# Performance work log

Hardware: AMD Instinct MI355X
Metric: run time of the kernel (lower is better)

The kernel has to match this reference:

```python
import jax, jax.numpy as jnp
import numpy as np


def _layernorm(x, g, b, eps=1e-5):
    mu = jnp.mean(x, axis=-1, keepdims=True)
    var = jnp.mean(jnp.square(x - mu), axis=-1, keepdims=True)
    return (x - mu) * jax.lax.rsqrt(var + eps) * g + b


def setup_inputs() -> dict:
    key = jax.random.key(0)
    ks = jax.random.split(key, 8)
    dim, ctx_dim, heads, dim_head = 256, 256, 8, 64
    inner = heads * dim_head
    s = 0.02
    return {
        "x": jax.random.normal(ks[0], (4, dim, 64, 64), jnp.float32),
        "y": jax.random.normal(ks[1], (4, 1024, ctx_dim), jnp.float32),
        "ln_x_g": jnp.ones((dim,), jnp.float32),
        "ln_x_b": jnp.zeros((dim,), jnp.float32),
        "ln_y_g": jnp.ones((ctx_dim,), jnp.float32),
        "ln_y_b": jnp.zeros((ctx_dim,), jnp.float32),
        "Wq": jax.random.normal(ks[2], (dim, inner), jnp.float32) * s,
        "Wk": jax.random.normal(ks[3], (ctx_dim, inner), jnp.float32) * s,
        "Wv": jax.random.normal(ks[4], (ctx_dim, inner), jnp.float32) * s,
        "bv": jnp.zeros((inner,), jnp.float32),
        "Wo": jax.random.normal(ks[5], (inner, dim), jnp.float32) * s,
        "bo": jnp.zeros((dim,), jnp.float32),
    }


def reference(x, y, ln_x_g, ln_x_b, ln_y_g, ln_y_b, Wq, Wk, Wv, bv, Wo, bo):
    heads, dim_head = 8, 64
    b, c = x.shape[:2]
    # channel_last=False path: [b, c, H, W] -> [b, n, c]
    xn = x.reshape(b, c, -1).swapaxes(1, 2)
    xn = _layernorm(xn, ln_x_g, ln_x_b)          # note: x is reassigned in torch code
    yn = _layernorm(y, ln_y_g, ln_y_b)
    q = xn @ Wq                                   # [b, n, h*d]
    k = yn @ Wk                                   # [b, m, h*d]
    v = yn @ Wv + bv                              # [b, m, h*d]

    def split_heads(t):
        B, N, _ = t.shape
        return t.reshape(B, N, heads, dim_head).transpose(0, 2, 1, 3)  # [b, h, n, d]

    q, k, v = split_heads(q), split_heads(k), split_heads(v)
    attn = jnp.einsum("bhid,bhjd->bhij", q, k) * (dim_head ** -0.5)
    attn = jax.nn.softmax(attn, axis=-1)
    out = jnp.einsum("bhij,bhjd->bhid", attn, v)  # [b, h, n, d]
    out = out.transpose(0, 2, 1, 3).reshape(b, -1, heads * dim_head)
    out = out @ Wo + bo
    return xn + out  # residual with layernormed x (faithful to source)
```

## Files before the change

kernel.cpp:

```cpp
#include <hip/hip_runtime.h>
#include <hip/hip_bf16.h>
#include <cstddef>
#include <cstdint>

#define BATCH 4
#define CDIM 256
#define HW 4096
#define MCTX 1024
#define CTX 256
#define HEADS 8
#define DHEAD 64
#define INNER 512

typedef __attribute__((ext_vector_type(8))) short bf16x8;
typedef __attribute__((ext_vector_type(4))) float f32x4;

static __device__ __forceinline__ ushort f2bf(float f) {
  __hip_bfloat16 h = __float2bfloat16(f);
  return *reinterpret_cast<ushort*>(&h);
}

static __device__ __forceinline__ void gload16(const void* g, void* l) {
  __builtin_amdgcn_global_load_lds(
      (const __attribute__((address_space(1))) void*)(uintptr_t)g,
      (__attribute__((address_space(3))) void*)(uint32_t)(uintptr_t)l,
      16, 0, 0);
}

__global__ __launch_bounds__(256) void ln_x_kernel(
    const float* __restrict__ x, const float* __restrict__ g,
    const float* __restrict__ bta, float* __restrict__ xn,
    ushort* __restrict__ xnbf) {
  const int blk = blockIdx.x;
  const int bi = blk / (HW / 32);
  const int n0 = (blk % (HW / 32)) * 32;
  __shared__ float xt[32][257];
  __shared__ float smu[32], srs[32];
  const int t = threadIdx.x;
  const float* xb = x + (size_t)bi * CDIM * HW;
  {
    const int cr = t >> 3;
    const int n4 = (t & 7) * 4;
    #pragma unroll
    for (int pass = 0; pass < 8; ++pass) {
      const int c = pass * 32 + cr;
      float4 v = *(const float4*)(xb + (size_t)c * HW + n0 + n4);
      xt[n4 + 0][c] = v.x; xt[n4 + 1][c] = v.y;
      xt[n4 + 2][c] = v.z; xt[n4 + 3][c] = v.w;
    }
  }
  __syncthreads();
  const int col = t >> 3, j = t & 7;
  float s = 0.f, ss = 0.f;
  #pragma unroll
  for (int c = j; c < CDIM; c += 8) {
    float v = xt[col][c];
    s += v; ss += v * v;
  }
  #pragma unroll
  for (int off = 1; off < 8; off <<= 1) {
    s += __shfl_xor(s, off);
    ss += __shfl_xor(ss, off);
  }
  if (j == 0) {
    float mu = s * (1.f / CDIM);
    smu[col] = mu;
    srs[col] = rsqrtf(ss * (1.f / CDIM) - mu * mu + 1e-5f);
  }
  __syncthreads();
  const float gv = g[t], bvv = bta[t];
  float* xnb = xn + ((size_t)bi * HW + n0) * CDIM;
  ushort* xbb = xnbf + ((size_t)bi * HW + n0) * CDIM;
  #pragma unroll 4
  for (int n = 0; n < 32; ++n) {
    float val = (xt[n][t] - smu[n]) * srs[n] * gv + bvv;
    xnb[(size_t)n * CDIM + t] = val;
    xbb[(size_t)n * CDIM + t] = f2bf(val);
  }
}

__global__ __launch_bounds__(256) void ln_y_kernel(
    const float* __restrict__ y, const float* __restrict__ g,
    const float* __restrict__ bta, ushort* __restrict__ ynbf) {
  const int row = blockIdx.x * 4 + (threadIdx.x >> 6);
  const int t = threadIdx.x & 63;
  float4 v = ((const float4*)(y + (size_t)row * CTX))[t];
  float s = v.x + v.y + v.z + v.w;
  float ss = v.x * v.x + v.y * v.y + v.z * v.z + v.w * v.w;
  #pragma unroll
  for (int off = 1; off < 64; off <<= 1) {
    s += __shfl_xor(s, off);
    ss += __shfl_xor(ss, off);
  }
  float mu = s * (1.f / CTX);
  float rs = rsqrtf(ss * (1.f / CTX) - mu * mu + 1e-5f);
  float4 gv = ((const float4*)g)[t];
  float4 b4 = ((const float4*)bta)[t];
  ushort4 ob;
  ob.x = f2bf((v.x - mu) * rs * gv.x + b4.x);
  ob.y = f2bf((v.y - mu) * rs * gv.y + b4.y);
  ob.z = f2bf((v.z - mu) * rs * gv.z + b4.z);
  ob.w = f2bf((v.w - mu) * rs * gv.w + b4.w);
  *(ushort4*)(ynbf + (size_t)row * CTX + t * 4) = ob;
}

static __device__ __forceinline__ void wprep_body(
    const float* __restrict__ W, ushort* __restrict__ Wt, int K, int N,
    int bx, int by) {
  __shared__ ushort T[64][65];
  const int k0 = by * 64, n0 = bx * 64;
  const int t = threadIdx.x;
  #pragma unroll
  for (int rr = 0; rr < 4; ++rr) {
    int row = rr * 16 + (t >> 4);
    int c = (t & 15) * 4;
    float4 wv = *(const float4*)(W + (size_t)(k0 + row) * N + n0 + c);
    T[row][c + 0] = f2bf(wv.x); T[row][c + 1] = f2bf(wv.y);
    T[row][c + 2] = f2bf(wv.z); T[row][c + 3] = f2bf(wv.w);
  }
  __syncthreads();
  #pragma unroll
  for (int rr = 0; rr < 4; ++rr) {
    int nrow = rr * 16 + (t >> 4);
    int kc = (t & 15) * 4;
    ushort4 o;
    o.x = T[kc + 0][nrow]; o.y = T[kc + 1][nrow];
    o.z = T[kc + 2][nrow]; o.w = T[kc + 3][nrow];
    *(ushort4*)(Wt + (size_t)(n0 + nrow) * K + k0 + kc) = o;
  }
}

__global__ __launch_bounds__(256) void wprep4_kernel(
    const float* __restrict__ W0, const float* __restrict__ W1,
    const float* __restrict__ W2, const float* __restrict__ W3,
    ushort* __restrict__ T0, ushort* __restrict__ T1,
    ushort* __restrict__ T2, ushort* __restrict__ T3) {
  const int z = blockIdx.z;
  if (z < 3) {
    const float* W = (z == 0) ? W0 : (z == 1) ? W1 : W2;
    ushort* Wt = (z == 0) ? T0 : (z == 1) ? T1 : T2;
    wprep_body(W, Wt, 256, 512, blockIdx.x, blockIdx.y);
  } else {
    wprep_body(W3, T3, 512, 256, blockIdx.x & 3,
               blockIdx.y * 2 + (blockIdx.x >> 2));
  }
}

template <bool F32_RES_OUT>
static __device__ __forceinline__ void gemm_body(
    const ushort* __restrict__ A, const ushort* __restrict__ Bt,
    const float* __restrict__ bias, const float* __restrict__ res,
    void* __restrict__ Cout, ushort* __restrict__ vt_out,
    int M, int N, int K, float scale, int m0, int n0) {
  __shared__ ushort As[128 * 64];
  __shared__ ushort Bs[128 * 64];
  const int t = threadIdx.x;
  const int l = t & 63, w = t >> 6;
  const int lq = l & 15, lg = l >> 4;
  const int wr = w >> 1, wc = w & 1;
  f32x4 acc[4][4];
  #pragma unroll
  for (int mt = 0; mt < 4; ++mt)
    #pragma unroll
    for (int nt = 0; nt < 4; ++nt)
      #pragma unroll
      for (int e = 0; e < 4; ++e) acc[mt][nt][e] = 0.f;
  const int srow = w * 8 + (l >> 3);
  const int scol = ((l & 7) ^ (l >> 3)) * 8;
  const ushort* pA = A + (size_t)(m0 + srow) * K + scol;
  const ushort* pB = Bt + (size_t)(n0 + srow) * K + scol;
  const int dbase = w * 512;
  for (int k0 = 0; k0 < K; k0 += 64) {
    if (k0) __syncthreads();
    #pragma unroll
    for (int i = 0; i < 4; ++i) {
      gload16(pA + (size_t)(i * 32) * K + k0, &As[i * 2048 + dbase]);
      gload16(pB + (size_t)(i * 32) * K + k0, &Bs[i * 2048 + dbase]);
    }
    __syncthreads();
    #pragma unroll
    for (int ks = 0; ks < 2; ++ks) {
      bf16x8 af[4], bfr[4];
      #pragma unroll
      for (int mt = 0; mt < 4; ++mt) {
        const int R = wr * 64 + mt * 16 + lq;
        af[mt] = *(const bf16x8*)(
            &As[R * 64 + ((ks * 32 + lg * 8) ^ ((R & 7) * 8))]);
      }
      #pragma unroll
      for (int nt = 0; nt < 4; ++nt) {
        const int R = wc * 64 + nt * 16 + lq;
        bfr[nt] = *(const bf16x8*)(
            &Bs[R * 64 + ((ks * 32 + lg * 8) ^ ((R & 7) * 8))]);
      }
      #pragma unroll
      for (int mt = 0; mt < 4; ++mt)
        #pragma unroll
        for (int nt = 0; nt < 4; ++nt)
          acc[mt][nt] = __builtin_amdgcn_mfma_f32_16x16x32_bf16(
              af[mt], bfr[nt], acc[mt][nt], 0, 0, 0);
    }
  }
  #pragma unroll
  for (int nt = 0; nt < 4; ++nt) {
    const int colc = n0 + wc * 64 + nt * 16 + lq;
    const float bcol = bias ? bias[colc] : 0.f;
    #pragma unroll
    for (int mt = 0; mt < 4; ++mt) {
      #pragma unroll
      for (int i = 0; i < 4; ++i) {
        const size_t row = (size_t)(m0 + wr * 64 + mt * 16 + lg * 4 + i);
        float v = acc[mt][nt][i] * scale + bcol;
        if (vt_out) {
          vt_out[(size_t)((((row >> 10) * 8 + (colc >> 6)) << 6) + (colc & 63)) * MCTX
                 + (row & (MCTX - 1))] = f2bf(v);
        } else if (F32_RES_OUT) {
          ((float*)Cout)[row * N + colc] = v + res[row * N + colc];
        } else {
          ((ushort*)Cout)[row * N + colc] = f2bf(v);
        }
      }
    }
  }
}

template <bool F32_RES_OUT>
__global__ __launch_bounds__(256) void mfma_gemm(
    const ushort* __restrict__ A, const ushort* __restrict__ Bt,
    const float* __restrict__ bias, const float* __restrict__ res,
    void* __restrict__ Cout, int M, int N, int K, float scale) {
  gemm_body<F32_RES_OUT>(A, Bt, bias, res, Cout, nullptr, M, N, K, scale,
                         blockIdx.y * 128, blockIdx.x * 128);
}

__global__ __launch_bounds__(256) void mfma_gemm_kv(
    const ushort* __restrict__ A, const ushort* __restrict__ BtK,
    const ushort* __restrict__ BtV, const float* __restrict__ bv,
    ushort* __restrict__ Ck, ushort* __restrict__ vt_out) {
  const bool isV = blockIdx.x >= 4;
  gemm_body<false>(A, isV ? BtV : BtK, isV ? bv : nullptr, nullptr,
                   (void*)Ck, isV ? vt_out : nullptr, 4096, 512, 256, 1.f,
                   blockIdx.y * 128, (blockIdx.x & 3) * 128);
}

__global__ __launch_bounds__(512, 4) void attn_mfma(
    const ushort* __restrict__ q, const ushort* __restrict__ k,
    const ushort* __restrict__ vt, ushort* __restrict__ ao) {
  const int bid = blockIdx.x + 16 * (blockIdx.y + 8 * blockIdx.z);
  const int swz = (bid & 7) * 64 + (bid >> 3);
  const int bi = swz >> 7;
  const int h = (swz >> 4) & 7;
  const int n0 = (swz & 15) * 256;
  const int tile0 = (bid & 3) << 2;
  __shared__ ushort Ks[2][64 * 64];
  __shared__ ushort Vs[2][64 * 64];
  __shared__ ushort Ps[8][2][16 * 64];
  const int t = threadIdx.x;
  const int l = t & 63, w = t >> 6;
  const int lq = l & 15, lg = l >> 4;

  bf16x8 bq[2][2];
  #pragma unroll
  for (int g = 0; g < 2; ++g) {
    const size_t qrow = (size_t)(bi * HW + n0 + w * 32 + g * 16 + lq);
    #pragma unroll
    for (int ks = 0; ks < 2; ++ks)
      bq[g][ks] = *(const bf16x8*)(q + qrow * INNER + h * DHEAD + ks * 32 + lg * 8);
  }

  float m_run[2] = {-1e30f, -1e30f}, l_run[2] = {0.f, 0.f};
  f32x4 oacc[2][4];
  #pragma unroll
  for (int g = 0; g < 2; ++g)
    #pragma unroll
    for (int dt = 0; dt < 4; ++dt)
      #pragma unroll
      for (int e = 0; e < 4; ++e) oacc[g][dt][e] = 0.f;

  const int rr = t >> 3, cc = (t & 7) * 8;
  const ushort* kptr = k + (size_t)(bi * MCTX + rr) * INNER + h * DHEAD + cc;
  const ushort* vptr = vt + (size_t)((bi * HEADS + h) * 64 + rr) * MCTX + cc;
  const int sidx = (rr * 64 + cc) ^ ((rr & 7) << 3);

  {
    const int ms = tile0 << 6;
    uint4 k0v = *(const uint4*)(kptr + (size_t)ms * INNER);
    uint4 v0v = *(const uint4*)(vptr + ms);
    *(uint4*)(&Ks[0][sidx]) = k0v;
    *(uint4*)(&Vs[0][sidx]) = v0v;
  }
  __syncthreads();

  auto softmax_group = [&](f32x4 (&scg)[4], float& mr, float& lr,
                           f32x4 (&oa)[4], ushort* psw) {
    f32x4 mv;
    #pragma unroll
    for (int e = 0; e < 4; ++e)
      mv[e] = fmaxf(fmaxf(scg[0][e], scg[1][e]), fmaxf(scg[2][e], scg[3][e]));
    float mloc = fmaxf(fmaxf(mv[0], mv[1]), fmaxf(mv[2], mv[3]));
    mloc = fmaxf(mloc, __shfl_xor(mloc, 16));
    mloc = fmaxf(mloc, __shfl_xor(mloc, 32));
    if (!__all((int)(mloc - mr <= 8.f))) {
      const float mnew = fmaxf(mr, mloc);
      const float corr = __builtin_amdgcn_exp2f(mr - mnew);
      lr *= corr;
      mr = mnew;
      #pragma unroll
      for (int i = 0; i < 4; ++i) {
        float ci = __shfl(corr, lg * 4 + i);
        #pragma unroll
        for (int dt = 0; dt < 4; ++dt) oa[dt][i] *= ci;
      }
    }
    #pragma unroll
    for (int j = 0; j < 4; ++j)
      #pragma unroll
      for (int e = 0; e < 4; ++e)
        scg[j][e] = __builtin_amdgcn_exp2f(scg[j][e] - mr);
    f32x4 s4;
    #pragma unroll
    for (int e = 0; e < 4; ++e)
      s4[e] = (scg[0][e] + scg[1][e]) + (scg[2][e] + scg[3][e]);
    float psum = (s4[0] + s4[1]) + (s4[2] + s4[3]);
    psum += __shfl_xor(psum, 16);
    psum += __shfl_xor(psum, 32);
    lr += psum;
    #pragma unroll
    for (int j = 0; j < 4; ++j) {
      uint2 pk;
      pk.x = (uint)f2bf(scg[j][0]) | ((uint)f2bf(scg[j][1]) << 16);
      pk.y = (uint)f2bf(scg[j][2]) | ((uint)f2bf(scg[j][3]) << 16);
      *(uint2*)(psw + ((lq * 64 + j * 16 + lg * 4) ^ ((lq & 7) << 3))) = pk;
    }
  };

  #pragma unroll 2
  for (int it = 0; it < 16; ++it) {
    const int buf = it & 1;
    const bool more = (it + 1) < 16;
    const int mnext = ((tile0 + it + 1) & 15) << 6;
    uint4 kpre{}, vpre{};
    if (more) {
      kpre = *(const uint4*)(kptr + (size_t)mnext * INNER);
      vpre = *(const uint4*)(vptr + mnext);
    }
    f32x4 sc[2][4];
    #pragma unroll
    for (int g = 0; g < 2; ++g)
      #pragma unroll
      for (int j = 0; j < 4; ++j)
        #pragma unroll
        for (int e = 0; e < 4; ++e) sc[g][j][e] = 0.f;
    __builtin_amdgcn_s_setprio(1);
    #pragma unroll
    for (int j = 0; j < 4; ++j) {
      #pragma unroll
      for (int ks = 0; ks < 2; ++ks) {
        const int krow = j * 16 + lq;
        bf16x8 ak = *(const bf16x8*)(
            &Ks[buf][(krow * 64 + ks * 32 + lg * 8) ^ ((krow & 7) << 3)]);
        sc[0][j] = __builtin_amdgcn_mfma_f32_16x16x32_bf16(ak, bq[0][ks], sc[0][j], 0, 0, 0);
        sc[1][j] = __builtin_amdgcn_mfma_f32_16x16x32_bf16(ak, bq[1][ks], sc[1][j], 0, 0, 0);
      }
    }
    __builtin_amdgcn_s_setprio(0);
    softmax_group(sc[0], m_run[0], l_run[0], oacc[0], &Ps[w][0][0]);
    if (more) {
      *(uint4*)(&Ks[buf ^ 1][sidx]) = kpre;
      *(uint4*)(&Vs[buf ^ 1][sidx]) = vpre;
    }
    softmax_group(sc[1], m_run[1], l_run[1], oacc[1], &Ps[w][1][0]);
    bf16x8 pa[2][2];
    #pragma unroll
    for (int g = 0; g < 2; ++g)
      #pragma unroll
      for (int ks = 0; ks < 2; ++ks)
        pa[g][ks] = *(const bf16x8*)(
            &Ps[w][g][(lq * 64 + ks * 32 + lg * 8) ^ ((lq & 7) << 3)]);
    __builtin_amdgcn_s_setprio(1);
    #pragma unroll
    for (int dt = 0; dt < 4; ++dt) {
      #pragma unroll
      for (int ks = 0; ks < 2; ++ks) {
        const int vrow = dt * 16 + lq;
        bf16x8 vb = *(const bf16x8*)(
            &Vs[buf][(vrow * 64 + ks * 32 + lg * 8) ^ ((vrow & 7) << 3)]);
        oacc[0][dt] = __builtin_amdgcn_mfma_f32_16x16x32_bf16(pa[0][ks], vb, oacc[0][dt], 0, 0, 0);
        oacc[1][dt] = __builtin_amdgcn_mfma_f32_16x16x32_bf16(pa[1][ks], vb, oacc[1][dt], 0, 0, 0);
      }
    }
    __builtin_amdgcn_s_setprio(0);
    __syncthreads();
  }
  #pragma unroll
  for (int g = 0; g < 2; ++g) {
    const float rl = 1.f / l_run[g];
    #pragma unroll
    for (int i = 0; i < 4; ++i) {
      float li = __shfl(rl, lg * 4 + i);
      const size_t row = (size_t)(bi * HW + n0 + w * 32 + g * 16 + lg * 4 + i);
      #pragma unroll
      for (int dt = 0; dt < 4; ++dt)
        ao[row * INNER + h * DHEAD + dt * 16 + lq] = f2bf(oacc[g][dt][i] * li);
    }
  }
}

extern "C" void kernel_launch(void* const* d_in, const int* in_sizes, int n_in,
                              void* d_out, int out_size, void* d_ws, size_t ws_size,
                              hipStream_t stream) {
  const float* x     = (const float*)d_in[0];
  const float* y     = (const float*)d_in[1];
  const float* ln_xg = (const float*)d_in[2];
  const float* ln_xb = (const float*)d_in[3];
  const float* ln_yg = (const float*)d_in[4];
  const float* ln_yb = (const float*)d_in[5];
  const float* Wq    = (const float*)d_in[6];
  const float* Wk    = (const float*)d_in[7];
  const float* Wv    = (const float*)d_in[8];
  const float* bv    = (const float*)d_in[9];
  const float* Wo    = (const float*)d_in[10];
  const float* bo    = (const float*)d_in[11];
  float* out = (float*)d_out;

  char* p = (char*)d_ws;
  float*  xn   = (float*)p;  p += (size_t)16384 * 256 * 4;
  ushort* xnbf = (ushort*)p; p += (size_t)16384 * 256 * 2;
  ushort* ynbf = (ushort*)p; p += (size_t)4096 * 256 * 2;
  ushort* wtq  = (ushort*)p; p += (size_t)512 * 256 * 2;
  ushort* wtk  = (ushort*)p; p += (size_t)512 * 256 * 2;
  ushort* wtv  = (ushort*)p; p += (size_t)512 * 256 * 2;
  ushort* wto  = (ushort*)p; p += (size_t)256 * 512 * 2;
  ushort* qbf  = (ushort*)p; p += (size_t)16384 * 512 * 2;
  ushort* kbf  = (ushort*)p; p += (size_t)4096 * 512 * 2;
  ushort* vtb  = (ushort*)p; p += (size_t)4096 * 512 * 2;
  ushort* aobf = (ushort*)p; p += (size_t)16384 * 512 * 2;

  wprep4_kernel<<<dim3(8, 4, 4), 256, 0, stream>>>(
      Wq, Wk, Wv, Wo, wtq, wtk, wtv, wto);
  ln_x_kernel<<<dim3(BATCH * (HW / 32)), 256, 0, stream>>>(x, ln_xg, ln_xb, xn, xnbf);
  ln_y_kernel<<<dim3(BATCH * MCTX / 4), 256, 0, stream>>>(y, ln_yg, ln_yb, ynbf);
  mfma_gemm<false><<<dim3(4, 128), 256, 0, stream>>>(
      xnbf, wtq, nullptr, nullptr, qbf, 16384, 512, 256, 0.1803368801111204f);
  mfma_gemm_kv<<<dim3(8, 32), 256, 0, stream>>>(ynbf, wtk, wtv, bv, kbf, vtb);
  attn_mfma<<<dim3(HW / 256, HEADS, BATCH), 512, 0, stream>>>(qbf, kbf, vtb, aobf);
  mfma_gemm<true><<<dim3(2, 128), 256, 0, stream>>>(
      aobf, wto, bo, xn, out, 16384, 256, 512, 1.f);
}
```

Measured before the change: 113.9 us.

## Switch attention to 32x32x16 MFMA and keep P in registers via permlane32 swap

```diff
diff --git a/kernel.cpp b/kernel.cpp
--- a/kernel.cpp
+++ b/kernel.cpp
@@ -14,6 +14,7 @@
 
 typedef __attribute__((ext_vector_type(8))) short bf16x8;
 typedef __attribute__((ext_vector_type(4))) float f32x4;
+typedef __attribute__((ext_vector_type(16))) float f32x16;
 
 static __device__ __forceinline__ ushort f2bf(float f) {
   __hip_bfloat16 h = __float2bfloat16(f);
@@ -254,28 +255,24 @@
   const int tile0 = (bid & 3) << 2;
   __shared__ ushort Ks[2][64 * 64];
   __shared__ ushort Vs[2][64 * 64];
-  __shared__ ushort Ps[8][2][16 * 64];
   const int t = threadIdx.x;
   const int l = t & 63, w = t >> 6;
-  const int lq = l & 15, lg = l >> 4;
-
-  bf16x8 bq[2][2];
-  #pragma unroll
-  for (int g = 0; g < 2; ++g) {
-    const size_t qrow = (size_t)(bi * HW + n0 + w * 32 + g * 16 + lq);
-    #pragma unroll
-    for (int ks = 0; ks < 2; ++ks)
-      bq[g][ks] = *(const bf16x8*)(q + qrow * INNER + h * DHEAD + ks * 32 + lg * 8);
-  }
-
-  float m_run[2] = {-1e30f, -1e30f}, l_run[2] = {0.f, 0.f};
-  f32x4 oacc[2][4];
-  #pragma unroll
-  for (int g = 0; g < 2; ++g)
-    #pragma unroll
-    for (int dt = 0; dt < 4; ++dt)
-      #pragma unroll
-      for (int e = 0; e < 4; ++e) oacc[g][dt][e] = 0.f;
+  const int lq32 = l & 31, hi = l >> 5;
+
+  bf16x8 bq[4];
+  {
+    const size_t qrow = (size_t)(bi * HW + n0 + w * 32 + lq32);
+    #pragma unroll
+    for (int ds = 0; ds < 4; ++ds)
+      bq[ds] = *(const bf16x8*)(q + qrow * INNER + h * DHEAD + ds * 16 + hi * 8);
+  }
+
+  float m_run = -1e30f, l_run = 0.f;
+  f32x16 oacc[2];
+  #pragma unroll
+  for (int dt = 0; dt < 2; ++dt)
+    #pragma unroll
+    for (int e = 0; e < 16; ++e) oacc[dt][e] = 0.f;
 
   const int rr = t >> 3, cc = (t & 7) * 8;
   const ushort* kptr = k + (size_t)(bi * MCTX + rr) * INNER + h * DHEAD + cc;
@@ -291,50 +288,6 @@
   }
   __syncthreads();
 
-  auto softmax_group = [&](f32x4 (&scg)[4], float& mr, float& lr,
-                           f32x4 (&oa)[4], ushort* psw) {
-    f32x4 mv;
-    #pragma unroll
-    for (int e = 0; e < 4; ++e)
-      mv[e] = fmaxf(fmaxf(scg[0][e], scg[1][e]), fmaxf(scg[2][e], scg[3][e]));
-    float mloc = fmaxf(fmaxf(mv[0], mv[1]), fmaxf(mv[2], mv[3]));
-    mloc = fmaxf(mloc, __shfl_xor(mloc, 16));
-    mloc = fmaxf(mloc, __shfl_xor(mloc, 32));
-    if (!__all((int)(mloc - mr <= 8.f))) {
-      const float mnew = fmaxf(mr, mloc);
-      const float corr = __builtin_amdgcn_exp2f(mr - mnew);
-      lr *= corr;
-      mr = mnew;
-      #pragma unroll
-      for (int i = 0; i < 4; ++i) {
-        float ci = __shfl(corr, lg * 4 + i);
-        #pragma unroll
-        for (int dt = 0; dt < 4; ++dt) oa[dt][i] *= ci;
-      }
-    }
-    #pragma unroll
-    for (int j = 0; j < 4; ++j)
-      #pragma unroll
-      for (int e = 0; e < 4; ++e)
-        scg[j][e] = __builtin_amdgcn_exp2f(scg[j][e] - mr);
-    f32x4 s4;
-    #pragma unroll
-    for (int e = 0; e < 4; ++e)
-      s4[e] = (scg[0][e] + scg[1][e]) + (scg[2][e] + scg[3][e]);
-    float psum = (s4[0] + s4[1]) + (s4[2] + s4[3]);
-    psum += __shfl_xor(psum, 16);
-    psum += __shfl_xor(psum, 32);
-    lr += psum;
-    #pragma unroll
-    for (int j = 0; j < 4; ++j) {
-      uint2 pk;
-      pk.x = (uint)f2bf(scg[j][0]) | ((uint)f2bf(scg[j][1]) << 16);
-      pk.y = (uint)f2bf(scg[j][2]) | ((uint)f2bf(scg[j][3]) << 16);
-      *(uint2*)(psw + ((lq * 64 + j * 16 + lg * 4) ^ ((lq & 7) << 3))) = pk;
-    }
-  };
-
-  #pragma unroll 2
   for (int it = 0; it < 16; ++it) {
     const int buf = it & 1;
     const bool more = (it + 1) < 16;
@@ -344,65 +297,105 @@
       kpre = *(const uint4*)(kptr + (size_t)mnext * INNER);
       vpre = *(const uint4*)(vptr + mnext);
     }
-    f32x4 sc[2][4];
-    #pragma unroll
-    for (int g = 0; g < 2; ++g)
-      #pragma unroll
-      for (int j = 0; j < 4; ++j)
-        #pragma unroll
-        for (int e = 0; e < 4; ++e) sc[g][j][e] = 0.f;
+    f32x16 sc[2];
+    #pragma unroll
+    for (int kt = 0; kt < 2; ++kt)
+      #pragma unroll
+      for (int e = 0; e < 16; ++e) sc[kt][e] = 0.f;
     __builtin_amdgcn_s_setprio(1);
     #pragma unroll
-    for (int j = 0; j < 4; ++j) {
-      #pragma unroll
-      for (int ks = 0; ks < 2; ++ks) {
-        const int krow = j * 16 + lq;
+    for (int kt = 0; kt < 2; ++kt) {
+      #pragma unroll
+      for (int ds = 0; ds < 4; ++ds) {
+        const int krow = kt * 32 + lq32;
         bf16x8 ak = *(const bf16x8*)(
-            &Ks[buf][(krow * 64 + ks * 32 + lg * 8) ^ ((krow & 7) << 3)]);
-        sc[0][j] = __builtin_amdgcn_mfma_f32_16x16x32_bf16(ak, bq[0][ks], sc[0][j], 0, 0, 0);
-        sc[1][j] = __builtin_amdgcn_mfma_f32_16x16x32_bf16(ak, bq[1][ks], sc[1][j], 0, 0, 0);
+            &Ks[buf][(krow * 64 + ds * 16 + hi * 8) ^ ((krow & 7) << 3)]);
+        sc[kt] = __builtin_amdgcn_mfma_f32_32x32x16_bf16(ak, bq[ds], sc[kt], 0, 0, 0);
       }
     }
     __builtin_amdgcn_s_setprio(0);
-    softmax_group(sc[0], m_run[0], l_run[0], oacc[0], &Ps[w][0][0]);
+    f32x16 mx;
+    #pragma unroll
+    for (int e = 0; e < 16; ++e) mx[e] = fmaxf(sc[0][e], sc[1][e]);
+    #pragma unroll
+    for (int e = 0; e < 8; ++e) mx[e] = fmaxf(mx[e], mx[e + 8]);
+    #pragma unroll
+    for (int e = 0; e < 4; ++e) mx[e] = fmaxf(mx[e], mx[e + 4]);
+    float mloc = fmaxf(fmaxf(mx[0], mx[1]), fmaxf(mx[2], mx[3]));
+    mloc = fmaxf(mloc, __shfl_xor(mloc, 32));
+    if (!__all((int)(mloc - m_run <= 8.f))) {
+      const float mnew = fmaxf(m_run, mloc);
+      const float corr = __builtin_amdgcn_exp2f(m_run - mnew);
+      l_run *= corr;
+      m_run = mnew;
+      #pragma unroll
+      for (int r = 0; r < 16; ++r) {
+        const int qrow = (r & 3) + 8 * (r >> 2) + 4 * hi;
+        float ci = __shfl(corr, qrow);
+        oacc[0][r] *= ci; oacc[1][r] *= ci;
+      }
+    }
+    #pragma unroll
+    for (int kt = 0; kt < 2; ++kt)
+      #pragma unroll
+      for (int e = 0; e < 16; ++e)
+        sc[kt][e] = __builtin_amdgcn_exp2f(sc[kt][e] - m_run);
+    f32x16 s16;
+    #pragma unroll
+    for (int e = 0; e < 16; ++e) s16[e] = sc[0][e] + sc[1][e];
+    #pragma unroll
+    for (int e = 0; e < 8; ++e) s16[e] += s16[e + 8];
+    #pragma unroll
+    for (int e = 0; e < 4; ++e) s16[e] += s16[e + 4];
+    float psum = (s16[0] + s16[1]) + (s16[2] + s16[3]);
+    psum += __shfl_xor(psum, 32);
+    l_run += psum;
+    bf16x8 pafr[4];
+    #pragma unroll
+    for (int kt = 0; kt < 2; ++kt) {
+      uint wa[4], wb[4];
+      #pragma unroll
+      for (int r4 = 0; r4 < 4; ++r4) {
+        wa[r4] = (uint)f2bf(sc[kt][4 * r4]) | ((uint)f2bf(sc[kt][4 * r4 + 1]) << 16);
+        wb[r4] = (uint)f2bf(sc[kt][4 * r4 + 2]) | ((uint)f2bf(sc[kt][4 * r4 + 3]) << 16);
+      }
+      #pragma unroll
+      for (int p2 = 0; p2 < 2; ++p2) {
+        uint Sa = wa[2 * p2], Da = wa[2 * p2 + 1];
+        uint Sb = wb[2 * p2], Db = wb[2 * p2 + 1];
+        asm volatile("v_permlane32_swap_b32 %0, %1" : "+v"(Da), "+v"(Sa));
+        asm volatile("v_permlane32_swap_b32 %0, %1" : "+v"(Db), "+v"(Sb));
+        uint4 fr;
+        fr.x = Sa; fr.y = Sb; fr.z = Da; fr.w = Db;
+        pafr[kt * 2 + p2] = *reinterpret_cast<bf16x8*>(&fr);
+      }
+    }
     if (more) {
       *(uint4*)(&Ks[buf ^ 1][sidx]) = kpre;
       *(uint4*)(&Vs[buf ^ 1][sidx]) = vpre;
     }
-    softmax_group(sc[1], m_run[1], l_run[1], oacc[1], &Ps[w][1][0]);
-    bf16x8 pa[2][2];
-    #pragma unroll
-    for (int g = 0; g < 2; ++g)
-      #pragma unroll
-      for (int ks = 0; ks < 2; ++ks)
-        pa[g][ks] = *(const bf16x8*)(
-            &Ps[w][g][(lq * 64 + ks * 32 + lg * 8) ^ ((lq & 7) << 3)]);
     __builtin_amdgcn_s_setprio(1);
     #pragma unroll
-    for (int dt = 0; dt < 4; ++dt) {
-      #pragma unroll
-      for (int ks = 0; ks < 2; ++ks) {
-        const int vrow = dt * 16 + lq;
+    for (int dt = 0; dt < 2; ++dt) {
+      const int vrow = dt * 32 + lq32;
+      #pragma unroll
+      for (int kt16 = 0; kt16 < 4; ++kt16) {
         bf16x8 vb = *(const bf16x8*)(
-            &Vs[buf][(vrow * 64 + ks * 32 + lg * 8) ^ ((vrow & 7) << 3)]);
-        oacc[0][dt] = __builtin_amdgcn_mfma_f32_16x16x32_bf16(pa[0][ks], vb, oacc[0][dt], 0, 0, 0);
-        oacc[1][dt] = __builtin_amdgcn_mfma_f32_16x16x32_bf16(pa[1][ks], vb, oacc[1][dt], 0, 0, 0);
+            &Vs[buf][(vrow * 64 + kt16 * 16 + hi * 8) ^ ((vrow & 7) << 3)]);
+        oacc[dt] = __builtin_amdgcn_mfma_f32_32x32x16_bf16(pafr[kt16], vb, oacc[dt], 0, 0, 0);
       }
     }
     __builtin_amdgcn_s_setprio(0);
     __syncthreads();
   }
-  #pragma unroll
-  for (int g = 0; g < 2; ++g) {
-    const float rl = 1.f / l_run[g];
-    #pragma unroll
-    for (int i = 0; i < 4; ++i) {
-      float li = __shfl(rl, lg * 4 + i);
-      const size_t row = (size_t)(bi * HW + n0 + w * 32 + g * 16 + lg * 4 + i);
-      #pragma unroll
-      for (int dt = 0; dt < 4; ++dt)
-        ao[row * INNER + h * DHEAD + dt * 16 + lq] = f2bf(oacc[g][dt][i] * li);
-    }
+  const float rl = 1.f / l_run;
+  #pragma unroll
+  for (int r = 0; r < 16; ++r) {
+    const int qrow = (r & 3) + 8 * (r >> 2) + 4 * hi;
+    float li = __shfl(rl, qrow);
+    const size_t row = (size_t)(bi * HW + n0 + w * 32 + qrow);
+    ao[row * INNER + h * DHEAD + lq32] = f2bf(oacc[0][r] * li);
+    ao[row * INNER + h * DHEAD + 32 + lq32] = f2bf(oacc[1][r] * li);
   }
 }
 
```

New measurement: 114.2 us. Within noise of the previous version (+0.2%).
